# Optimization experiments

Hardware: AMD Instinct MI355X
Metric: run time of the kernel (lower is better)

The kernel has to match this reference:

```python
import jax, jax.numpy as jnp
import numpy as np

N = 65536          # total nodes
E = 131072         # total edges
G = 4096           # number of graphs (sessions)
NODES_PER_GRAPH = 16
H = 128            # hidden_dim
D = 64             # embedding_dim
NUM_ITEMS = 50000
NUM_CAT, NUM_SUB, NUM_EL, NUM_BR = 1000, 5000, 10000, 2000
NUM_ITERATIONS = 1


def setup_inputs() -> dict:
    key = jax.random.key(0)
    ks = jax.random.split(key, 24)
    inp = {
        "category": jax.random.randint(ks[0], (N,), 0, NUM_CAT),
        "sub_category": jax.random.randint(ks[1], (N,), 0, NUM_SUB),
        "element": jax.random.randint(ks[2], (N,), 0, NUM_EL),
        "brand": jax.random.randint(ks[3], (N,), 0, NUM_BR),
        "product_id": jax.random.randint(ks[4], (N,), 0, NUM_ITEMS),
        "price": jax.random.uniform(ks[5], (N, 1), dtype=jnp.float32),
        "edge_index": jax.random.randint(ks[6], (2, E), 0, N),
        "batch": jnp.arange(N) // NODES_PER_GRAPH,  # sorted node->graph ids
    }
    s = 0.05
    IN = 5 * D + 1  # 321
    inp["emb_cat"] = jax.random.normal(ks[7], (NUM_CAT, D), jnp.float32) * s
    inp["emb_sub"] = jax.random.normal(ks[8], (NUM_SUB, D), jnp.float32) * s
    inp["emb_el"] = jax.random.normal(ks[9], (NUM_EL, D), jnp.float32) * s
    inp["emb_br"] = jax.random.normal(ks[10], (NUM_BR, D), jnp.float32) * s
    inp["emb_item"] = jax.random.normal(ks[11], (NUM_ITEMS, D), jnp.float32) * s
    inp["Wm"] = jax.random.normal(ks[12], (H, IN), jnp.float32) * s
    inp["bm"] = jnp.zeros((H,), jnp.float32)
    inp["W_ih"] = jax.random.normal(ks[13], (3 * H, H), jnp.float32) * s
    inp["b_ih"] = jnp.zeros((3 * H,), jnp.float32)
    inp["W_hh"] = jax.random.normal(ks[14], (3 * H, H), jnp.float32) * s
    inp["b_hh"] = jnp.zeros((3 * H,), jnp.float32)
    inp["Wg1"] = jax.random.normal(ks[15], (H, H), jnp.float32) * s
    inp["bg1"] = jnp.zeros((H,), jnp.float32)
    inp["Wg2"] = jax.random.normal(ks[16], (1, H), jnp.float32) * s
    inp["bg2"] = jnp.zeros((1,), jnp.float32)
    inp["Wfc"] = jax.random.normal(ks[17], (NUM_ITEMS, H), jnp.float32) * s
    inp["bfc"] = jnp.zeros((NUM_ITEMS,), jnp.float32)
    return inp


def _forward(category, sub_category, element, brand, product_id, price,
             edge_index, batch, emb_cat, emb_sub, emb_el, emb_br, emb_item,
             Wm, bm, W_ih, b_ih, W_hh, b_hh, Wg1, bg1, Wg2, bg2, Wfc, bfc):
    # NodeEmbedding: concat of 5 lookups, then prepend price -> (N, 5D+1)
    emb = jnp.concatenate([
        emb_cat[category], emb_sub[sub_category], emb_el[element],
        emb_br[brand], emb_item[product_id]], axis=1)
    x = jnp.concatenate([price, emb], axis=1)

    # message_linear
    h = x @ Wm.T + bm  # (N, H)

    src, dst = edge_index[0], edge_index[1]  # source -> target
    for _ in range(NUM_ITERATIONS):
        # scatter-mean aggregation of source node embeddings at targets
        msg_sum = jax.ops.segment_sum(h[src], dst, num_segments=N)
        cnt = jax.ops.segment_sum(jnp.ones((E,), h.dtype), dst, num_segments=N)
        m = msg_sum / jnp.maximum(cnt, 1.0)[:, None]
        # GRUCell(m, h), PyTorch gate layout [r, z, n]
        gi = m @ W_ih.T + b_ih
        gh = h @ W_hh.T + b_hh
        gi_r, gi_z, gi_n = jnp.split(gi, 3, axis=1)
        gh_r, gh_z, gh_n = jnp.split(gh, 3, axis=1)
        r = jax.nn.sigmoid(gi_r + gh_r)
        z = jax.nn.sigmoid(gi_z + gh_z)
        n = jnp.tanh(gi_n + r * gh_n)
        h = (1.0 - z) * n + z * h

    # attentional aggregation: segment softmax over batch
    gate = (jax.nn.relu(h @ Wg1.T + bg1) @ Wg2.T + bg2)[:, 0]  # (N,)
    seg_max = jax.ops.segment_max(gate, batch, num_segments=G)
    alpha = jnp.exp(gate - seg_max[batch])
    denom = jax.ops.segment_sum(alpha, batch, num_segments=G)
    w = alpha / denom[batch]
    pooled = jax.ops.segment_sum(w[:, None] * h, batch, num_segments=G)  # (G, H)

    return pooled @ Wfc.T + bfc  # (G, num_items)


def reference(category, sub_category, element, brand, product_id, price,
              edge_index, batch, emb_cat, emb_sub, emb_el, emb_br, emb_item,
              Wm, bm, W_ih, b_ih, W_hh, b_hh, Wg1, bg1, Wg2, bg2, Wfc, bfc):
    return _forward(category, sub_category, element, brand, product_id, price,
                    edge_index, batch, emb_cat, emb_sub, emb_el, emb_br, emb_item,
                    Wm, bm, W_ih, b_ih, W_hh, b_hh, Wg1, bg1, Wg2, bg2, Wfc, bfc)
```

## Files before the change

kernel.cpp:

```cpp
#include <hip/hip_runtime.h>
#include <hip/hip_bf16.h>
#include <cstdint>
#include <cstddef>

#define NN 65536
#define EE 131072
#define GG 4096
#define HH 128
#define DD 64
#define KP 384
#define ITEMS 50000

typedef __attribute__((ext_vector_type(8))) short bf16x8;
typedef __attribute__((ext_vector_type(4))) float f32x4;
typedef unsigned short u16;
typedef __attribute__((ext_vector_type(4))) unsigned short u16x4;

#define PINV(x) asm volatile("" : "+v"(x))

__device__ inline void split2(float x, u16* hi, u16* lo) {
    __hip_bfloat16 h = __float2bfloat16(x);
    float hf = __bfloat162float(h);
    __hip_bfloat16 l = __float2bfloat16(x - hf);
    *hi = *reinterpret_cast<u16*>(&h);
    *lo = *reinterpret_cast<u16*>(&l);
}
__device__ inline u16 hi_only(float x) {
    __hip_bfloat16 h = __float2bfloat16(x);
    return *reinterpret_cast<u16*>(&h);
}
__device__ inline float bf2f(u16 v) {
    unsigned int u = ((unsigned int)v) << 16;
    return *reinterpret_cast<float*>(&u);
}

__global__ void k_embed(const int* __restrict__ cat, const int* __restrict__ sub,
                        const int* __restrict__ el, const int* __restrict__ br,
                        const int* __restrict__ pid, const float* __restrict__ price,
                        const float* __restrict__ ecat, const float* __restrict__ esub,
                        const float* __restrict__ eel, const float* __restrict__ ebr,
                        const float* __restrict__ eitem, u16* __restrict__ Xhi) {
    int tid = threadIdx.x;
    int n = blockIdx.x * 4 + (tid >> 6);
    int l = tid & 63;
    u16* xh = Xhi + (size_t)n * KP;
    if (l == 0) xh[0] = hi_only(price[n]);
    xh[1 + l]   = hi_only(ecat[(size_t)cat[n] * DD + l]);
    xh[65 + l]  = hi_only(esub[(size_t)sub[n] * DD + l]);
    xh[129 + l] = hi_only(eel [(size_t)el[n]  * DD + l]);
    xh[193 + l] = hi_only(ebr [(size_t)br[n]  * DD + l]);
    xh[257 + l] = hi_only(eitem[(size_t)pid[n]* DD + l]);
    if (l < 63) xh[321 + l] = 0;
}

__global__ void k_cvt_hi(const float* __restrict__ src, u16* __restrict__ hi, int n_total) {
    int i = blockIdx.x * 256 + threadIdx.x;
    if (i >= n_total) return;
    hi[i] = hi_only(src[i]);
}

__global__ void k_cvt_wm(const float* __restrict__ Wm, u16* __restrict__ hi) {
    int i = blockIdx.x * 256 + threadIdx.x;
    int r = i / KP, c = i - r * KP;
    float x = (c < 321) ? Wm[r * 321 + c] : 0.f;
    hi[i] = hi_only(x);
}

#define M1_STR 132
__launch_bounds__(256, 2)
__global__ void k_mlp1(const u16* __restrict__ Xhi, const u16* __restrict__ Whi,
                       const float* __restrict__ bm, float* __restrict__ h,
                       u16* __restrict__ hhi) {
    __shared__ float ls[128 * M1_STR];
    int tid = threadIdx.x, w = tid >> 6, l = tid & 63;
    int lr = l & 15, lk = l >> 4;
    int m0 = blockIdx.x * 128;
    f32x4 acc[2][8];
    #pragma unroll
    for (int rt = 0; rt < 2; ++rt)
        #pragma unroll
        for (int ci = 0; ci < 8; ++ci) acc[rt][ci] = (f32x4){0.f, 0.f, 0.f, 0.f};

    for (int kc = 0; kc < 12; ++kc) {
        bf16x8 ah[2];
        #pragma unroll
        for (int rt = 0; rt < 2; ++rt) {
            size_t off = (size_t)(m0 + w * 32 + rt * 16 + lr) * KP + kc * 32 + lk * 8;
            ah[rt] = *(const bf16x8*)(Xhi + off);
        }
        #pragma unroll
        for (int ci = 0; ci < 8; ++ci) {
            size_t boff = (size_t)(ci * 16 + lr) * KP + kc * 32 + lk * 8;
            bf16x8 bh = *(const bf16x8*)(Whi + boff);
            #pragma unroll
            for (int rt = 0; rt < 2; ++rt)
                acc[rt][ci] = __builtin_amdgcn_mfma_f32_16x16x32_bf16(ah[rt], bh, acc[rt][ci], 0, 0, 0);
        }
    }
    #pragma unroll
    for (int rt = 0; rt < 2; ++rt)
        #pragma unroll
        for (int ci = 0; ci < 8; ++ci) {
            int col = ci * 16 + lr;
            float bv = bm[col];
            #pragma unroll
            for (int q = 0; q < 4; ++q)
                ls[(w * 32 + rt * 16 + lk * 4 + q) * M1_STR + col] = acc[rt][ci][q] + bv;
        }
    __syncthreads();
    int row = tid >> 1, cb = (tid & 1) * 64;
    float* hd = h + (size_t)(m0 + row) * HH + cb;
    u16* hh = hhi + (size_t)(m0 + row) * HH + cb;
    #pragma unroll
    for (int i = 0; i < 64; i += 4) {
        float4 v = *(const float4*)&ls[row * M1_STR + cb + i];
        *(float4*)(hd + i) = v;
        u16x4 vh;
        vh.x = hi_only(v.x); vh.y = hi_only(v.y);
        vh.z = hi_only(v.z); vh.w = hi_only(v.w);
        *(u16x4*)(hh + i) = vh;
    }
}

__global__ void k_scatter(const u16* __restrict__ hhi, const int* __restrict__ edge,
                          float* __restrict__ msg, float* __restrict__ cnt) {
    int j = threadIdx.x & 127;
    int eo = threadIdx.x >> 7;
    int e0 = blockIdx.x * 16;
    #pragma unroll
    for (int it = 0; it < 8; ++it) {
        int e = e0 + it * 2 + eo;
        int s = edge[e];
        int d = edge[EE + e];
        atomicAdd(&msg[(size_t)d * HH + j], bf2f(hhi[(size_t)s * HH + j]));
        if (j == 0) atomicAdd(&cnt[d], 1.0f);
    }
}

#define GRU_STR 136
__launch_bounds__(256, 2)
__global__ void k_gru(const float* __restrict__ msg, const float* __restrict__ cnt,
                      const u16* __restrict__ hhi_in,
                      const u16* __restrict__ Wihh, const u16* __restrict__ Whhh,
                      const float* __restrict__ b_ih, const float* __restrict__ b_hh,
                      float* __restrict__ h, u16* __restrict__ hhi) {
    __shared__ float ls[32 * GRU_STR];
    int tid = threadIdx.x, w = tid >> 6, l = tid & 63;
    int lr = l & 15, lk = l >> 4;
    int m0 = blockIdx.x * 32;
    f32x4 acc[6][2][2];
    #pragma unroll
    for (int g = 0; g < 6; ++g)
        #pragma unroll
        for (int ct = 0; ct < 2; ++ct)
            #pragma unroll
            for (int rt = 0; rt < 2; ++rt) acc[g][ct][rt] = (f32x4){0.f, 0.f, 0.f, 0.f};

    float cinv[2];
    const float* mrow[2];
    #pragma unroll
    for (int rt = 0; rt < 2; ++rt) {
        int row = m0 + rt * 16 + lr;
        cinv[rt] = 1.0f / fmaxf(cnt[row], 1.0f);
        mrow[rt] = msg + (size_t)row * HH + lk * 8;
    }

    for (int kc = 0; kc < 4; ++kc) {
        bf16x8 amh[2], ahh[2];
        #pragma unroll
        for (int rt = 0; rt < 2; ++rt) {
            float4 v0 = *(const float4*)(mrow[rt] + kc * 32);
            float4 v1 = *(const float4*)(mrow[rt] + kc * 32 + 4);
            float xs[8] = {v0.x * cinv[rt], v0.y * cinv[rt], v0.z * cinv[rt], v0.w * cinv[rt],
                           v1.x * cinv[rt], v1.y * cinv[rt], v1.z * cinv[rt], v1.w * cinv[rt]};
            #pragma unroll
            for (int q = 0; q < 8; ++q) amh[rt][q] = (short)hi_only(xs[q]);
            size_t off = (size_t)(m0 + rt * 16 + lr) * HH + kc * 32 + lk * 8;
            ahh[rt] = *(const bf16x8*)(hhi_in + off);
        }
        #pragma unroll
        for (int g = 0; g < 6; ++g) {
            const u16* WH = (g < 3) ? Wihh : Whhh;
            int gb = (g % 3) * HH;
            #pragma unroll
            for (int ct = 0; ct < 2; ++ct) {
                size_t boff = (size_t)(gb + w * 32 + ct * 16 + lr) * HH + kc * 32 + lk * 8;
                bf16x8 bh = *(const bf16x8*)(WH + boff);
                #pragma unroll
                for (int rt = 0; rt < 2; ++rt) {
                    bf16x8 ah = (g < 3) ? amh[rt] : ahh[rt];
                    acc[g][ct][rt] = __builtin_amdgcn_mfma_f32_16x16x32_bf16(ah, bh, acc[g][ct][rt], 0, 0, 0);
                }
            }
        }
    }
    #pragma unroll
    for (int ct = 0; ct < 2; ++ct) {
        int col = w * 32 + ct * 16 + lr;
        float bir = b_ih[col], biz = b_ih[HH + col], bin = b_ih[2 * HH + col];
        float bhr = b_hh[col], bhz = b_hh[HH + col], bhn = b_hh[2 * HH + col];
        #pragma unroll
        for (int rt = 0; rt < 2; ++rt)
            #pragma unroll
            for (int q = 0; q < 4; ++q) {
                int rl = rt * 16 + lk * 4 + q;
                float gir = acc[0][ct][rt][q] + bir;
                float giz = acc[1][ct][rt][q] + biz;
                float gin = acc[2][ct][rt][q] + bin;
                float ghr = acc[3][ct][rt][q] + bhr;
                float ghz = acc[4][ct][rt][q] + bhz;
                float ghn = acc[5][ct][rt][q] + bhn;
                float hv = h[(size_t)(m0 + rl) * HH + col];
                float r = 1.f / (1.f + expf(-(gir + ghr)));
                float z = 1.f / (1.f + expf(-(giz + ghz)));
                float nn = tanhf(gin + r * ghn);
                ls[rl * GRU_STR + col] = (1.f - z) * nn + z * hv;
            }
    }
    __syncthreads();
    int row = tid >> 3, cb = (tid & 7) * 16;
    float* hd = h + (size_t)(m0 + row) * HH + cb;
    u16* hh = hhi + (size_t)(m0 + row) * HH + cb;
    #pragma unroll
    for (int i = 0; i < 16; i += 4) {
        float4 v = *(const float4*)&ls[row * GRU_STR + cb + i];
        *(float4*)(hd + i) = v;
        u16x4 vh;
        vh.x = hi_only(v.x); vh.y = hi_only(v.y);
        vh.z = hi_only(v.z); vh.w = hi_only(v.w);
        *(u16x4*)(hh + i) = vh;
    }
}

__launch_bounds__(256, 2)
__global__ void k_gatepool(const u16* __restrict__ hhi, const float* __restrict__ h,
                           const u16* __restrict__ Ghi, const float* __restrict__ bg1,
                           const float* __restrict__ Wg2,
                           u16* __restrict__ phi, u16* __restrict__ plo) {
    __shared__ float sal[128];
    int tid = threadIdx.x, w = tid >> 6, l = tid & 63;
    int lr = l & 15, lk = l >> 4;
    int m0 = blockIdx.x * 128;
    f32x4 acc[2][8];
    #pragma unroll
    for (int rt = 0; rt < 2; ++rt)
        #pragma unroll
        for (int ci = 0; ci < 8; ++ci) acc[rt][ci] = (f32x4){0.f, 0.f, 0.f, 0.f};

    for (int kc = 0; kc < 4; ++kc) {
        bf16x8 ah[2];
        #pragma unroll
        for (int rt = 0; rt < 2; ++rt) {
            size_t off = (size_t)(m0 + w * 32 + rt * 16 + lr) * HH + kc * 32 + lk * 8;
            ah[rt] = *(const bf16x8*)(hhi + off);
        }
        #pragma unroll
        for (int ci = 0; ci < 8; ++ci) {
            size_t boff = (size_t)(ci * 16 + lr) * HH + kc * 32 + lk * 8;
            bf16x8 bh = *(const bf16x8*)(Ghi + boff);
            #pragma unroll
            for (int rt = 0; rt < 2; ++rt)
                acc[rt][ci] = __builtin_amdgcn_mfma_f32_16x16x32_bf16(ah[rt], bh, acc[rt][ci], 0, 0, 0);
        }
    }
    float part[2][4] = {};
    #pragma unroll
    for (int ci = 0; ci < 8; ++ci) {
        int col = ci * 16 + lr;
        float wv = Wg2[col], bb = bg1[col];
        #pragma unroll
        for (int rt = 0; rt < 2; ++rt)
            #pragma unroll
            for (int q = 0; q < 4; ++q)
                part[rt][q] += fmaxf(acc[rt][ci][q] + bb, 0.f) * wv;
    }
    #pragma unroll
    for (int rt = 0; rt < 2; ++rt)
        #pragma unroll
        for (int q = 0; q < 4; ++q) {
            float v = part[rt][q];
            v += __shfl_xor(v, 1);
            v += __shfl_xor(v, 2);
            v += __shfl_xor(v, 4);
            v += __shfl_xor(v, 8);
            part[rt][q] = v;
        }
    if (lr == 0) {
        #pragma unroll
        for (int rt = 0; rt < 2; ++rt)
            #pragma unroll
            for (int q = 0; q < 4; ++q)
                sal[w * 32 + rt * 16 + lk * 4 + q] = part[rt][q];
    }
    __syncthreads();

    int g2 = tid >> 5;
    int c = (tid & 31) * 4;
    int rb = g2 * 16;
    float gv[16];
    float mx = -1e30f;
    #pragma unroll
    for (int i = 0; i < 16; ++i) { gv[i] = sal[rb + i]; mx = fmaxf(mx, gv[i]); }
    float den = 0.f;
    #pragma unroll
    for (int i = 0; i < 16; ++i) { gv[i] = expf(gv[i] - mx); den += gv[i]; }
    float inv = 1.f / den;
    f32x4 a = (f32x4){0.f, 0.f, 0.f, 0.f};
    #pragma unroll
    for (int i = 0; i < 16; ++i) {
        float4 hv = *(const float4*)&h[(size_t)(m0 + rb + i) * HH + c];
        float wgt = gv[i] * inv;
        a[0] += wgt * hv.x; a[1] += wgt * hv.y; a[2] += wgt * hv.z; a[3] += wgt * hv.w;
    }
    size_t po = (size_t)(blockIdx.x * 8 + g2) * HH + c;
    u16x4 vh, vl;
    #pragma unroll
    for (int q = 0; q < 4; ++q) split2(a[q], (u16*)&vh + q, (u16*)&vl + q);
    *(u16x4*)(phi + po) = vh;
    *(u16x4*)(plo + po) = vl;
}

#define FC_STR 520
__launch_bounds__(256, 2)
__global__ void k_fc12(const float* __restrict__ Wfc,
                       const u16* __restrict__ phi, const u16* __restrict__ plo,
                       const float* __restrict__ bfc, float* __restrict__ out) {
    __shared__ float ls[2][16][FC_STR];
    int wg = blockIdx.x;
    int xcd = wg & 7;
    int r = wg >> 3;
    int strip = (r >> 2) * 8 + xcd;
    int phase = r & 3;
    if (strip >= 98) return;
    int tid = threadIdx.x, w = tid >> 6, l = tid & 63;
    int lr = l & 15, lk = l >> 4;
    int c0 = strip * 512;
    int mbase = phase * 1024;

    bf16x8 bh[8][4];
    float bias[8];
    #pragma unroll
    for (int ci = 0; ci < 8; ++ci) {
        int n = c0 + w * 128 + ci * 16 + lr;
        bool ok = (n < ITEMS);
        const float* Wr = Wfc + (size_t)n * HH;
        #pragma unroll
        for (int kc = 0; kc < 4; ++kc) {
            float4 v0 = ok ? *(const float4*)(Wr + kc * 32 + lk * 8)     : make_float4(0.f,0.f,0.f,0.f);
            float4 v1 = ok ? *(const float4*)(Wr + kc * 32 + lk * 8 + 4) : make_float4(0.f,0.f,0.f,0.f);
            float xs[8] = {v0.x, v0.y, v0.z, v0.w, v1.x, v1.y, v1.z, v1.w};
            bf16x8 hv;
            #pragma unroll
            for (int q = 0; q < 8; ++q) hv[q] = (short)hi_only(xs[q]);
            bh[ci][kc] = hv;
        }
        bias[ci] = ok ? bfc[n] : 0.f;
    }
    #pragma unroll
    for (int ci = 0; ci < 8; ++ci)
        #pragma unroll
        for (int kc = 0; kc < 4; ++kc) PINV(bh[ci][kc]);

    bf16x8 a0h[4], a0l[4], a1h[4], a1l[4];
    auto LOADA = [&](int t, bf16x8* Ah, bf16x8* Al) {
        int m0 = mbase + t * 16;
        size_t aoff = (size_t)(m0 + lr) * HH + lk * 8;
        #pragma unroll
        for (int kc = 0; kc < 4; ++kc) {
            Ah[kc] = *(const bf16x8*)(phi + aoff + kc * 32);
            Al[kc] = *(const bf16x8*)(plo + aoff + kc * 32);
        }
    };
    auto COMP = [&](const bf16x8* Ah, const bf16x8* Al, int b) {
        #pragma unroll
        for (int ci = 0; ci < 8; ++ci) {
            f32x4 acc = (f32x4){0.f, 0.f, 0.f, 0.f};
            #pragma unroll
            for (int kc = 0; kc < 4; ++kc) {
                acc = __builtin_amdgcn_mfma_f32_16x16x32_bf16(Ah[kc], bh[ci][kc], acc, 0, 0, 0);
                acc = __builtin_amdgcn_mfma_f32_16x16x32_bf16(Al[kc], bh[ci][kc], acc, 0, 0, 0);
            }
            #pragma unroll
            for (int q = 0; q < 4; ++q)
                ls[b][lk * 4 + q][w * 128 + ci * 16 + lr] = acc[q] + bias[ci];
        }
    };
    auto FLUSH = [&](int t, int b) {
        int m0 = mbase + t * 16;
        #pragma unroll
        for (int p = 0; p < 4; ++p) {
            int row = w * 4 + p;
            #pragma unroll
            for (int s = 0; s < 2; ++s) {
                int c = s * 256 + l * 4;
                int gc = c0 + c;
                if (gc < ITEMS) {
                    f32x4 v = *(const f32x4*)&ls[b][row][c];
                    __builtin_nontemporal_store(v, (f32x4*)&out[(size_t)(m0 + row) * ITEMS + gc]);
                }
            }
        }
    };
    auto softbar = [&]() {
        asm volatile("s_waitcnt lgkmcnt(0)" ::: "memory");
        __builtin_amdgcn_s_barrier();
    };

    LOADA(0, a0h, a0l);
    LOADA(1, a1h, a1l);
    COMP(a0h, a0l, 0);
    softbar();
    for (int t = 1; t < 64; ++t) {
        if (t + 1 < 64) {
            if ((t + 1) & 1) LOADA(t + 1, a1h, a1l);
            else             LOADA(t + 1, a0h, a0l);
        }
        if (t & 1) COMP(a1h, a1l, 1);
        else       COMP(a0h, a0l, 0);
        FLUSH(t - 1, (t - 1) & 1);
        softbar();
    }
    FLUSH(63, 1);
}

extern "C" void kernel_launch(void* const* d_in, const int* in_sizes, int n_in,
                              void* d_out, int out_size, void* d_ws, size_t ws_size,
                              hipStream_t stream) {
    const int* category = (const int*)d_in[0];
    const int* sub_cat  = (const int*)d_in[1];
    const int* element  = (const int*)d_in[2];
    const int* brand    = (const int*)d_in[3];
    const int* pid      = (const int*)d_in[4];
    const float* price  = (const float*)d_in[5];
    const int* edge     = (const int*)d_in[6];
    const float* ecat   = (const float*)d_in[8];
    const float* esub   = (const float*)d_in[9];
    const float* eel    = (const float*)d_in[10];
    const float* ebr    = (const float*)d_in[11];
    const float* eitem  = (const float*)d_in[12];
    const float* Wm     = (const float*)d_in[13];
    const float* bm     = (const float*)d_in[14];
    const float* W_ih   = (const float*)d_in[15];
    const float* b_ih   = (const float*)d_in[16];
    const float* W_hh   = (const float*)d_in[17];
    const float* b_hh   = (const float*)d_in[18];
    const float* Wg1    = (const float*)d_in[19];
    const float* bg1    = (const float*)d_in[20];
    const float* Wg2    = (const float*)d_in[21];
    const float* Wfc    = (const float*)d_in[23];
    const float* bfc    = (const float*)d_in[24];
    float* out = (float*)d_out;

    char* p = (char*)d_ws;
    auto alloc = [&](size_t bytes) { char* r = p; p += (bytes + 255) & ~(size_t)255; return r; };
    u16* Xhi   = (u16*)alloc((size_t)NN * KP * 2);
    float* h   = (float*)alloc((size_t)NN * HH * 4);
    u16* hhi   = (u16*)alloc((size_t)NN * HH * 2);
    float* msg = (float*)alloc((size_t)NN * HH * 4);
    float* cnt = (float*)alloc((size_t)NN * 4);
    u16* phi   = (u16*)alloc((size_t)GG * HH * 2);
    u16* plo   = (u16*)alloc((size_t)GG * HH * 2);
    u16* Wmhi  = (u16*)alloc((size_t)HH * KP * 2);
    u16* Wihhi = (u16*)alloc((size_t)3 * HH * HH * 2);
    u16* Whhhi = (u16*)alloc((size_t)3 * HH * HH * 2);
    u16* Wg1hi = (u16*)alloc((size_t)HH * HH * 2);

    hipMemsetAsync(msg, 0, (size_t)NN * HH * sizeof(float), stream);
    hipMemsetAsync(cnt, 0, (size_t)NN * sizeof(float), stream);

    k_cvt_wm<<<(HH * KP + 255) / 256, 256, 0, stream>>>(Wm, Wmhi);
    k_cvt_hi<<<(3 * HH * HH + 255) / 256, 256, 0, stream>>>(W_ih, Wihhi, 3 * HH * HH);
    k_cvt_hi<<<(3 * HH * HH + 255) / 256, 256, 0, stream>>>(W_hh, Whhhi, 3 * HH * HH);
    k_cvt_hi<<<(HH * HH + 255) / 256, 256, 0, stream>>>(Wg1, Wg1hi, HH * HH);

    k_embed<<<NN / 4, 256, 0, stream>>>(category, sub_cat, element, brand, pid, price,
                                        ecat, esub, eel, ebr, eitem, Xhi);
    k_mlp1<<<NN / 128, 256, 0, stream>>>(Xhi, Wmhi, bm, h, hhi);
    k_scatter<<<EE / 16, 256, 0, stream>>>(hhi, edge, msg, cnt);
    k_gru<<<NN / 32, 256, 0, stream>>>(msg, cnt, hhi, Wihhi, Whhhi,
                                       b_ih, b_hh, h, hhi);
    k_gatepool<<<NN / 128, 256, 0, stream>>>(hhi, h, Wg1hi, bg1, Wg2, phi, plo);
    k_fc12<<<dim3(416), 256, 0, stream>>>(Wfc, phi, plo, bfc, out);
}
```

Measured before the change: 442.7 us.

## Store hidden state as bf16 hi/lo pair and pre-convert Wfc to padded bf16

Replaces the fp32 hidden-state buffer with two bf16 planes (hi and lo) that MLP1, GRU and gatepool write and read, which removes one fp32 store/load round trip per stage while keeping roughly fp32 precision. Wfc is now converted once to a zero-padded bf16 buffer by a separate kernel, so the FC kernel loads bf16 directly without bounds checks or per-element conversion. The catch is an extra conversion launch that reads all of Wfc and writes a new buffer, and GRU now reads hhi in place while also writing it.

```diff
diff --git a/kernel.cpp b/kernel.cpp
--- a/kernel.cpp
+++ b/kernel.cpp
@@ -10,6 +10,7 @@
 #define DD 64
 #define KP 384
 #define ITEMS 50000
+#define NPAD 50176
 
 typedef __attribute__((ext_vector_type(8))) short bf16x8;
 typedef __attribute__((ext_vector_type(4))) float f32x4;
@@ -53,10 +54,11 @@
     if (l < 63) xh[321 + l] = 0;
 }
 
-__global__ void k_cvt_hi(const float* __restrict__ src, u16* __restrict__ hi, int n_total) {
+__global__ void k_cvt_hi(const float* __restrict__ src, u16* __restrict__ hi,
+                         int n_valid, int n_total) {
     int i = blockIdx.x * 256 + threadIdx.x;
     if (i >= n_total) return;
-    hi[i] = hi_only(src[i]);
+    hi[i] = (i < n_valid) ? hi_only(src[i]) : (u16)0;
 }
 
 __global__ void k_cvt_wm(const float* __restrict__ Wm, u16* __restrict__ hi) {
@@ -69,8 +71,8 @@
 #define M1_STR 132
 __launch_bounds__(256, 2)
 __global__ void k_mlp1(const u16* __restrict__ Xhi, const u16* __restrict__ Whi,
-                       const float* __restrict__ bm, float* __restrict__ h,
-                       u16* __restrict__ hhi) {
+                       const float* __restrict__ bm,
+                       u16* __restrict__ hhi, u16* __restrict__ hlo) {
     __shared__ float ls[128 * M1_STR];
     int tid = threadIdx.x, w = tid >> 6, l = tid & 63;
     int lr = l & 15, lk = l >> 4;
@@ -109,16 +111,18 @@
         }
     __syncthreads();
     int row = tid >> 1, cb = (tid & 1) * 64;
-    float* hd = h + (size_t)(m0 + row) * HH + cb;
     u16* hh = hhi + (size_t)(m0 + row) * HH + cb;
+    u16* hl = hlo + (size_t)(m0 + row) * HH + cb;
     #pragma unroll
     for (int i = 0; i < 64; i += 4) {
         float4 v = *(const float4*)&ls[row * M1_STR + cb + i];
-        *(float4*)(hd + i) = v;
-        u16x4 vh;
-        vh.x = hi_only(v.x); vh.y = hi_only(v.y);
-        vh.z = hi_only(v.z); vh.w = hi_only(v.w);
+        u16x4 vh, vl;
+        split2(v.x, (u16*)&vh + 0, (u16*)&vl + 0);
+        split2(v.y, (u16*)&vh + 1, (u16*)&vl + 1);
+        split2(v.z, (u16*)&vh + 2, (u16*)&vl + 2);
+        split2(v.w, (u16*)&vh + 3, (u16*)&vl + 3);
         *(u16x4*)(hh + i) = vh;
+        *(u16x4*)(hl + i) = vl;
     }
 }
 
@@ -140,10 +144,9 @@
 #define GRU_STR 136
 __launch_bounds__(256, 2)
 __global__ void k_gru(const float* __restrict__ msg, const float* __restrict__ cnt,
-                      const u16* __restrict__ hhi_in,
                       const u16* __restrict__ Wihh, const u16* __restrict__ Whhh,
                       const float* __restrict__ b_ih, const float* __restrict__ b_hh,
-                      float* __restrict__ h, u16* __restrict__ hhi) {
+                      u16* __restrict__ hhi, u16* __restrict__ hlo) {
     __shared__ float ls[32 * GRU_STR];
     int tid = threadIdx.x, w = tid >> 6, l = tid & 63;
     int lr = l & 15, lk = l >> 4;
@@ -176,7 +179,7 @@
             #pragma unroll
             for (int q = 0; q < 8; ++q) amh[rt][q] = (short)hi_only(xs[q]);
             size_t off = (size_t)(m0 + rt * 16 + lr) * HH + kc * 32 + lk * 8;
-            ahh[rt] = *(const bf16x8*)(hhi_in + off);
+            ahh[rt] = *(const bf16x8*)(hhi + off);
         }
         #pragma unroll
         for (int g = 0; g < 6; ++g) {
@@ -204,13 +207,14 @@
             #pragma unroll
             for (int q = 0; q < 4; ++q) {
                 int rl = rt * 16 + lk * 4 + q;
+                size_t idx = (size_t)(m0 + rl) * HH + col;
                 float gir = acc[0][ct][rt][q] + bir;
                 float giz = acc[1][ct][rt][q] + biz;
                 float gin = acc[2][ct][rt][q] + bin;
                 float ghr = acc[3][ct][rt][q] + bhr;
                 float ghz = acc[4][ct][rt][q] + bhz;
                 float ghn = acc[5][ct][rt][q] + bhn;
-                float hv = h[(size_t)(m0 + rl) * HH + col];
+                float hv = bf2f(hhi[idx]) + bf2f(hlo[idx]);
                 float r = 1.f / (1.f + expf(-(gir + ghr)));
                 float z = 1.f / (1.f + expf(-(giz + ghz)));
                 float nn = tanhf(gin + r * ghn);
@@ -219,21 +223,23 @@
     }
     __syncthreads();
     int row = tid >> 3, cb = (tid & 7) * 16;
-    float* hd = h + (size_t)(m0 + row) * HH + cb;
     u16* hh = hhi + (size_t)(m0 + row) * HH + cb;
+    u16* hl = hlo + (size_t)(m0 + row) * HH + cb;
     #pragma unroll
     for (int i = 0; i < 16; i += 4) {
         float4 v = *(const float4*)&ls[row * GRU_STR + cb + i];
-        *(float4*)(hd + i) = v;
-        u16x4 vh;
-        vh.x = hi_only(v.x); vh.y = hi_only(v.y);
-        vh.z = hi_only(v.z); vh.w = hi_only(v.w);
+        u16x4 vh, vl;
+        split2(v.x, (u16*)&vh + 0, (u16*)&vl + 0);
+        split2(v.y, (u16*)&vh + 1, (u16*)&vl + 1);
+        split2(v.z, (u16*)&vh + 2, (u16*)&vl + 2);
+        split2(v.w, (u16*)&vh + 3, (u16*)&vl + 3);
         *(u16x4*)(hh + i) = vh;
+        *(u16x4*)(hl + i) = vl;
     }
 }
 
 __launch_bounds__(256, 2)
-__global__ void k_gatepool(const u16* __restrict__ hhi, const float* __restrict__ h,
+__global__ void k_gatepool(const u16* __restrict__ hhi, const u16* __restrict__ hlo,
                            const u16* __restrict__ Ghi, const float* __restrict__ bg1,
                            const float* __restrict__ Wg2,
                            u16* __restrict__ phi, u16* __restrict__ plo) {
@@ -308,9 +314,14 @@
     f32x4 a = (f32x4){0.f, 0.f, 0.f, 0.f};
     #pragma unroll
     for (int i = 0; i < 16; ++i) {
-        float4 hv = *(const float4*)&h[(size_t)(m0 + rb + i) * HH + c];
+        size_t idx = (size_t)(m0 + rb + i) * HH + c;
+        u16x4 xh = *(const u16x4*)(hhi + idx);
+        u16x4 xl = *(const u16x4*)(hlo + idx);
         float wgt = gv[i] * inv;
-        a[0] += wgt * hv.x; a[1] += wgt * hv.y; a[2] += wgt * hv.z; a[3] += wgt * hv.w;
+        a[0] += wgt * (bf2f(xh.x) + bf2f(xl.x));
+        a[1] += wgt * (bf2f(xh.y) + bf2f(xl.y));
+        a[2] += wgt * (bf2f(xh.z) + bf2f(xl.z));
+        a[3] += wgt * (bf2f(xh.w) + bf2f(xl.w));
     }
     size_t po = (size_t)(blockIdx.x * 8 + g2) * HH + c;
     u16x4 vh, vl;
@@ -322,7 +333,7 @@
 
 #define FC_STR 520
 __launch_bounds__(256, 2)
-__global__ void k_fc12(const float* __restrict__ Wfc,
+__global__ void k_fc13(const u16* __restrict__ Wfcb,
                        const u16* __restrict__ phi, const u16* __restrict__ plo,
                        const float* __restrict__ bfc, float* __restrict__ out) {
     __shared__ float ls[2][16][FC_STR];
@@ -342,19 +353,11 @@
     #pragma unroll
     for (int ci = 0; ci < 8; ++ci) {
         int n = c0 + w * 128 + ci * 16 + lr;
-        bool ok = (n < ITEMS);
-        const float* Wr = Wfc + (size_t)n * HH;
-        #pragma unroll
-        for (int kc = 0; kc < 4; ++kc) {
-            float4 v0 = ok ? *(const float4*)(Wr + kc * 32 + lk * 8)     : make_float4(0.f,0.f,0.f,0.f);
-            float4 v1 = ok ? *(const float4*)(Wr + kc * 32 + lk * 8 + 4) : make_float4(0.f,0.f,0.f,0.f);
-            float xs[8] = {v0.x, v0.y, v0.z, v0.w, v1.x, v1.y, v1.z, v1.w};
-            bf16x8 hv;
-            #pragma unroll
-            for (int q = 0; q < 8; ++q) hv[q] = (short)hi_only(xs[q]);
-            bh[ci][kc] = hv;
-        }
-        bias[ci] = ok ? bfc[n] : 0.f;
+        const u16* Wr = Wfcb + (size_t)n * HH + lk * 8;
+        #pragma unroll
+        for (int kc = 0; kc < 4; ++kc)
+            bh[ci][kc] = *(const bf16x8*)(Wr + kc * 32);
+        bias[ci] = (n < ITEMS) ? bfc[n] : 0.f;
     }
     #pragma unroll
     for (int ci = 0; ci < 8; ++ci)
@@ -454,8 +457,8 @@
     char* p = (char*)d_ws;
     auto alloc = [&](size_t bytes) { char* r = p; p += (bytes + 255) & ~(size_t)255; return r; };
     u16* Xhi   = (u16*)alloc((size_t)NN * KP * 2);
-    float* h   = (float*)alloc((size_t)NN * HH * 4);
     u16* hhi   = (u16*)alloc((size_t)NN * HH * 2);
+    u16* hlo   = (u16*)alloc((size_t)NN * HH * 2);
     float* msg = (float*)alloc((size_t)NN * HH * 4);
     float* cnt = (float*)alloc((size_t)NN * 4);
     u16* phi   = (u16*)alloc((size_t)GG * HH * 2);
@@ -464,21 +467,22 @@
     u16* Wihhi = (u16*)alloc((size_t)3 * HH * HH * 2);
     u16* Whhhi = (u16*)alloc((size_t)3 * HH * HH * 2);
     u16* Wg1hi = (u16*)alloc((size_t)HH * HH * 2);
+    u16* Wfcb  = (u16*)alloc((size_t)NPAD * HH * 2);
 
     hipMemsetAsync(msg, 0, (size_t)NN * HH * sizeof(float), stream);
     hipMemsetAsync(cnt, 0, (size_t)NN * sizeof(float), stream);
 
     k_cvt_wm<<<(HH * KP + 255) / 256, 256, 0, stream>>>(Wm, Wmhi);
-    k_cvt_hi<<<(3 * HH * HH + 255) / 256, 256, 0, stream>>>(W_ih, Wihhi, 3 * HH * HH);
-    k_cvt_hi<<<(3 * HH * HH + 255) / 256, 256, 0, stream>>>(W_hh, Whhhi, 3 * HH * HH);
-    k_cvt_hi<<<(HH * HH + 255) / 256, 256, 0, stream>>>(Wg1, Wg1hi, HH * HH);
+    k_cvt_hi<<<(3 * HH * HH + 255) / 256, 256, 0, stream>>>(W_ih, Wihhi, 3 * HH * HH, 3 * HH * HH);
+    k_cvt_hi<<<(3 * HH * HH + 255) / 256, 256, 0, stream>>>(W_hh, Whhhi, 3 * HH * HH, 3 * HH * HH);
+    k_cvt_hi<<<(HH * HH + 255) / 256, 256, 0, stream>>>(Wg1, Wg1hi, HH * HH, HH * HH);
+    k_cvt_hi<<<(NPAD * HH + 255) / 256, 256, 0, stream>>>(Wfc, Wfcb, ITEMS * HH, NPAD * HH);
 
     k_embed<<<NN / 4, 256, 0, stream>>>(category, sub_cat, element, brand, pid, price,
                                         ecat, esub, eel, ebr, eitem, Xhi);
-    k_mlp1<<<NN / 128, 256, 0, stream>>>(Xhi, Wmhi, bm, h, hhi);
+    k_mlp1<<<NN / 128, 256, 0, stream>>>(Xhi, Wmhi, bm, hhi, hlo);
     k_scatter<<<EE / 16, 256, 0, stream>>>(hhi, edge, msg, cnt);
-    k_gru<<<NN / 32, 256, 0, stream>>>(msg, cnt, hhi, Wihhi, Whhhi,
-                                       b_ih, b_hh, h, hhi);
-    k_gatepool<<<NN / 128, 256, 0, stream>>>(hhi, h, Wg1hi, bg1, Wg2, phi, plo);
-    k_fc12<<<dim3(416), 256, 0, stream>>>(Wfc, phi, plo, bfc, out);
-}
+    k_gru<<<NN / 32, 256, 0, stream>>>(msg, cnt, Wihhi, Whhhi, b_ih, b_hh, hhi, hlo);
+    k_gatepool<<<NN / 128, 256, 0, stream>>>(hhi, hlo, Wg1hi, bg1, Wg2, phi, plo);
+    k_fc13<<<dim3(416), 256, 0, stream>>>(Wfcb, phi, plo, bfc, out);
+}
```

After: 423.5 us. 1.05x faster.
